# Performance work log

Measured on AMD Instinct MI355X. Metric: run time of the kernel, lower is better.

The kernel has to match this reference:

```python
import jax, jax.numpy as jnp
import numpy as np

N_NODES = 16384
N_EDGES = 32768
D = 128          # node feature / hidden dim
EDGE_DIM = 10    # bond featurizer one-hot dim
EH = 32          # edge_hidden_dim in the NNConv MLPs


def _nnconv(x, src, dst, edge_attr, l1w, l1b, l2w, l2b, root, bias):
    """PyG NNConv with aggr='mean': out_i = x_i @ root + mean_{e: dst=i} x_{src_e} @ W(e) + bias."""
    E = edge_attr.shape[0]
    h = jax.nn.relu(edge_attr @ l1w + l1b)              # [E, EH]
    W = (h @ l2w + l2b).reshape(E, D, D)                # per-edge weight matrices [E, D, D]
    msg = jnp.einsum('ei,eio->eo', x[src], W)           # gather + per-edge matmul [E, D]
    s = jax.ops.segment_sum(msg, dst, num_segments=N_NODES)
    cnt = jax.ops.segment_sum(jnp.ones((E, 1), x.dtype), dst, num_segments=N_NODES)
    agg = s / jnp.maximum(cnt, 1.0)                     # scatter-mean (0 for isolated nodes)
    return x @ root + agg + bias


def setup_inputs() -> dict:
    key = jax.random.key(0)
    ks = jax.random.split(key, 14)
    x = jax.random.normal(ks[0], (N_NODES, D), dtype=jnp.float32)
    edge_index = jax.random.randint(ks[1], (2, N_EDGES), 0, N_NODES, dtype=jnp.int64)
    edge_attr = jax.random.uniform(ks[2], (N_EDGES, EDGE_DIM), dtype=jnp.float32)

    def lin(k, fan_in, fan_out):
        return jax.random.normal(k, (fan_in, fan_out), dtype=jnp.float32) / np.sqrt(fan_in)

    return {
        'x': x, 'edge_index': edge_index, 'edge_attr': edge_attr,
        # subgraph_conv1 (128 -> 128)
        'w1_l1': lin(ks[3], EDGE_DIM, EH), 'b1_l1': jnp.zeros((EH,), jnp.float32),
        'w1_l2': lin(ks[4], EH, D * D),    'b1_l2': jnp.zeros((D * D,), jnp.float32),
        'w1_root': lin(ks[5], D, D),       'b1': jnp.zeros((D,), jnp.float32),
        # subgraph_conv2 (128 -> 128), applied twice with shared weights
        'w2_l1': lin(ks[6], EDGE_DIM, EH), 'b2_l1': jnp.zeros((EH,), jnp.float32),
        'w2_l2': lin(ks[7], EH, D * D),    'b2_l2': jnp.zeros((D * D,), jnp.float32),
        'w2_root': lin(ks[8], D, D),       'b2': jnp.zeros((D,), jnp.float32),
    }


def reference(x, edge_index, edge_attr,
              w1_l1, b1_l1, w1_l2, b1_l2, w1_root, b1,
              w2_l1, b2_l1, w2_l2, b2_l2, w2_root, b2):
    src, dst = edge_index[0], edge_index[1]
    h = jax.nn.relu(_nnconv(x, src, dst, edge_attr, w1_l1, b1_l1, w1_l2, b1_l2, w1_root, b1))
    h = jax.nn.relu(_nnconv(h, src, dst, edge_attr, w2_l1, b2_l1, w2_l2, b2_l2, w2_root, b2))
    h = _nnconv(h, src, dst, edge_attr, w2_l1, b2_l1, w2_l2, b2_l2, w2_root, b2)
    return h
```

## Files before the change

kernel.cpp:

```cpp
#include <hip/hip_runtime.h>

#define N_NODES 16384
#define N_EDGES 32768
#define D 128
#define EDGE_DIM 10
#define KH 32
#define BM 128
#define XST 136
#define NBL 32

typedef _Float16 f16;
typedef _Float16 f16x4 __attribute__((ext_vector_type(4)));
typedef _Float16 f16x8 __attribute__((ext_vector_type(8)));
typedef float f32x4 __attribute__((ext_vector_type(4)));

__global__ __launch_bounds__(256) void deg_count_kernel(
    const int* __restrict__ ei, int* __restrict__ deg) {
  int e = blockIdx.x * blockDim.x + threadIdx.x;
  if (e < N_EDGES) atomicAdd(&deg[ei[N_EDGES + e]], 1);
}

__global__ __launch_bounds__(1024) void scan_kernel(
    const int* __restrict__ deg, int* __restrict__ rs, int* __restrict__ fill) {
  __shared__ int part[1024];
  int t = threadIdx.x;
  int base = t * 16;
  int loc[16], s = 0;
#pragma unroll
  for (int j = 0; j < 16; j++) { loc[j] = deg[base + j]; s += loc[j]; }
  part[t] = s;
  __syncthreads();
  for (int off = 1; off < 1024; off <<= 1) {
    int add = (t >= off) ? part[t - off] : 0;
    __syncthreads();
    part[t] += add;
    __syncthreads();
  }
  int run = t ? part[t - 1] : 0;
#pragma unroll
  for (int j = 0; j < 16; j++) {
    rs[base + j] = run; fill[base + j] = run; run += loc[j];
  }
  if (t == 1023) rs[N_NODES] = run;
}

__global__ __launch_bounds__(256) void scatter_mlp_kernel(
    const int* __restrict__ ei, const float* __restrict__ ea,
    int* __restrict__ fill,
    const float* __restrict__ w1l1, const float* __restrict__ b1l1,
    const float* __restrict__ w2l1, const float* __restrict__ b2l1,
    int* __restrict__ srcs, f16* __restrict__ h1, f16* __restrict__ h2) {
  int e = blockIdx.x * blockDim.x + threadIdx.x;
  if (e >= N_EDGES) return;
  int pos = atomicAdd(&fill[ei[N_EDGES + e]], 1);
  srcs[pos] = ei[e];
  float a[EDGE_DIM];
#pragma unroll
  for (int d = 0; d < EDGE_DIM; d++) a[d] = ea[e * EDGE_DIM + d];
  f16 hv1[KH], hv2[KH];
#pragma unroll
  for (int k = 0; k < KH; k++) {
    float acc1 = b1l1[k], acc2 = b2l1[k];
#pragma unroll
    for (int d = 0; d < EDGE_DIM; d++) {
      acc1 += a[d] * w1l1[d * KH + k];
      acc2 += a[d] * w2l1[d * KH + k];
    }
    hv1[k] = (f16)fmaxf(acc1, 0.0f);
    hv2[k] = (f16)fmaxf(acc2, 0.0f);
  }
  f16x8* d1 = (f16x8*)(h1 + (size_t)pos * KH);
  f16x8* d2 = (f16x8*)(h2 + (size_t)pos * KH);
#pragma unroll
  for (int c = 0; c < 4; c++) {
    d1[c] = *(f16x8*)&hv1[c * 8];
    d2[c] = *(f16x8*)&hv2[c * 8];
  }
}

__global__ __launch_bounds__(256) void pack_all_kernel(
    const float* __restrict__ w1l2, const float* __restrict__ w2l2,
    const float* __restrict__ b1l2, const float* __restrict__ b2l2,
    const float* __restrict__ rt1, const float* __restrict__ rt2,
    f16* __restrict__ Bp1, f16* __restrict__ Bp2,
    f16* __restrict__ Rp1, f16* __restrict__ Rp2) {
  int y = blockIdx.y;
  int t = blockIdx.x * 256 + threadIdx.x;
  if (y < 2) {
    const float* l2w = y ? w2l2 : w1l2;
    f16* Bp = y ? Bp2 : Bp1;
    f16 tmp[KH];
#pragma unroll
    for (int k = 0; k < KH; k++) tmp[k] = (f16)l2w[(size_t)k * (D * D) + t];
    f16x8* dst = (f16x8*)(Bp + (size_t)t * KH);
#pragma unroll
    for (int c = 0; c < 4; c++) dst[c] = *(f16x8*)&tmp[c * 8];
  } else {
    const float* src = (y == 2) ? b1l2 : (y == 3) ? b2l2 : (y == 4) ? rt1 : rt2;
    f16* dst = (y == 2) ? (Bp1 + (size_t)D * D * KH)
             : (y == 3) ? (Bp2 + (size_t)D * D * KH)
             : (y == 4) ? Rp1 : Rp2;
    int i = t >> 7, o = t & 127;
    dst[((size_t)(i >> 5) * D + o) * KH + (i & 31)] = (f16)src[t];
  }
}

__global__ __launch_bounds__(256, 2) void msg_mfma_kernel(
    const float* __restrict__ xin, const f16* __restrict__ hf,
    const f16* __restrict__ Bp, const int* __restrict__ srcs,
    f16* __restrict__ msgf) {
  __shared__ f16 Xs[BM][XST];
  __shared__ f16 Hs[BM][KH];
  int t = threadIdx.x;
  int e0 = blockIdx.x * BM;

  ((f16x8*)Hs)[t] = ((const f16x8*)(hf + (size_t)e0 * KH))[t];
  ((f16x8*)Hs)[t + 256] = ((const f16x8*)(hf + (size_t)e0 * KH))[t + 256];
  {
    int r = t >> 1, q = t & 1;
    int s = srcs[e0 + r];
    const float4* src = (const float4*)(xin + (size_t)s * D + q * 64);
    f16* dst = &Xs[r][q * 64];
#pragma unroll
    for (int c = 0; c < 16; c++) {
      float4 v = src[c];
      f16x4 h4 = {(f16)v.x, (f16)v.y, (f16)v.z, (f16)v.w};
      *(f16x4*)(dst + c * 4) = h4;
    }
  }

  int L = t & 63, w = t >> 6;
  int quad = L >> 4, lm = L & 15;
  int n0 = blockIdx.y * 64 + w * 16;

  const f16* bl = Bp + (size_t)(n0 + lm) * KH + quad * 8;
  const size_t istr = (size_t)D * KH;

  f32x4 acc[8];
#pragma unroll
  for (int mt = 0; mt < 8; mt++) acc[mt] = (f32x4){0.f, 0.f, 0.f, 0.f};

  f16x8 bufA[8], bufB[8];

  auto loadg = [&](f16x8 (&buf)[8], int basei) {
#pragma unroll
    for (int jj = 0; jj < 8; jj++)
      buf[jj] = *(const f16x8*)(bl + (size_t)(basei + jj) * istr);
  };

  f16x8 hreg[8];

  auto compute = [&](f16x8 (&buf)[8], int ig) {
    f16x8 xv[8];
#pragma unroll
    for (int mt = 0; mt < 8; mt++)
      xv[mt] = *(const f16x8*)&Xs[mt * 16 + lm][ig];
#pragma unroll
    for (int jj = 0; jj < 8; jj++) {
#pragma unroll
      for (int mt = 0; mt < 8; mt++) {
        f16 xs = xv[mt][jj];
        f16x8 xb = {xs, xs, xs, xs, xs, xs, xs, xs};
        f16x8 a = hreg[mt] * xb;
        acc[mt] = __builtin_amdgcn_mfma_f32_16x16x32_f16(a, buf[jj], acc[mt], 0, 0, 0);
      }
    }
  };

  loadg(bufA, 0);
  __syncthreads();

#pragma unroll
  for (int mt = 0; mt < 8; mt++)
    hreg[mt] = *(const f16x8*)&Hs[mt * 16 + lm][quad * 8];

#pragma unroll 1
  for (int g = 0; g < 8; g++) {
    loadg(bufB, 16 * g + 8);
    compute(bufA, 16 * g);
    loadg(bufA, 16 * g + 16);
    compute(bufB, 16 * g + 8);
  }

#pragma unroll
  for (int ig2 = 0; ig2 < 4; ig2++) {
#pragma unroll
    for (int mt = 0; mt < 8; mt++) {
      f16x8 a = *(const f16x8*)&Xs[mt * 16 + lm][ig2 * 32 + quad * 8];
      acc[mt] = __builtin_amdgcn_mfma_f32_16x16x32_f16(a, bufA[ig2], acc[mt], 0, 0, 0);
    }
  }

#pragma unroll
  for (int mt = 0; mt < 8; mt++)
#pragma unroll
    for (int r = 0; r < 4; r++)
      msgf[(size_t)(e0 + mt * 16 + quad * 4 + r) * D + n0 + lm] = (f16)acc[mt][r];
}

__global__ __launch_bounds__(256) void node_update_kernel(
    const float* __restrict__ xin, const f16* __restrict__ msgf,
    const int* __restrict__ rs, const f16* __restrict__ Rp,
    const float* __restrict__ bias, float* __restrict__ out, int do_relu) {
  __shared__ f16 Xs[NBL][XST];
  __shared__ float Sls[NBL][D];
  int t = threadIdx.x;
  int nb = blockIdx.x * NBL;

  {
    int r = t >> 3, q = t & 7;
    const float4* src = (const float4*)(xin + (size_t)(nb + r) * D + q * 16);
    f16* dst = &Xs[r][q * 16];
#pragma unroll
    for (int c = 0; c < 4; c++) {
      float4 v = src[c];
      f16x4 h4 = {(f16)v.x, (f16)v.y, (f16)v.z, (f16)v.w};
      *(f16x4*)(dst + c * 4) = h4;
    }
  }
  __syncthreads();

  {
    int nl = t >> 3, o0 = (t & 7) * 16;
    int n = nb + nl;
    int a = rs[n], b = rs[n + 1];
    float sum[16];
#pragma unroll
    for (int j = 0; j < 16; j++) sum[j] = 0.f;
    for (int r = a; r < b; r++) {
      f16x8 v0 = *(const f16x8*)(msgf + (size_t)r * D + o0);
      f16x8 v1 = *(const f16x8*)(msgf + (size_t)r * D + o0 + 8);
#pragma unroll
      for (int j = 0; j < 8; j++) {
        sum[j] += (float)v0[j];
        sum[8 + j] += (float)v1[j];
      }
    }
    float inv = 1.0f / (float)max(b - a, 1);
#pragma unroll
    for (int j = 0; j < 16; j++) Sls[nl][o0 + j] = sum[j] * inv;
  }
  __syncthreads();

  int L = t & 63, w = t >> 6;
  int quad = L >> 4, lm = L & 15;
  int n0 = w * 32;
  f32x4 acc[2][2];
#pragma unroll
  for (int mt = 0; mt < 2; mt++)
#pragma unroll
    for (int nt = 0; nt < 2; nt++)
      acc[mt][nt] = (f32x4){0.f, 0.f, 0.f, 0.f};
#pragma unroll
  for (int s4 = 0; s4 < 4; s4++) {
    const f16* b2l = Rp + ((size_t)s4 * D + n0 + lm) * KH + quad * 8;
    f16x8 b0 = *(const f16x8*)b2l;
    f16x8 b1 = *(const f16x8*)(b2l + 16 * KH);
#pragma unroll
    for (int mt = 0; mt < 2; mt++) {
      f16x8 a = *(const f16x8*)&Xs[mt * 16 + lm][s4 * 32 + quad * 8];
      acc[mt][0] = __builtin_amdgcn_mfma_f32_16x16x32_f16(a, b0, acc[mt][0], 0, 0, 0);
      acc[mt][1] = __builtin_amdgcn_mfma_f32_16x16x32_f16(a, b1, acc[mt][1], 0, 0, 0);
    }
  }
#pragma unroll
  for (int mt = 0; mt < 2; mt++)
#pragma unroll
    for (int r = 0; r < 4; r++) {
      Sls[mt * 16 + quad * 4 + r][n0 + lm] += acc[mt][0][r];
      Sls[mt * 16 + quad * 4 + r][n0 + 16 + lm] += acc[mt][1][r];
    }
  __syncthreads();

  {
    int o = t & 127, g = t >> 7;
    float bo = bias[o];
    for (int q = g * 16; q < g * 16 + 16; q++) {
      float v = bo + Sls[q][o];
      out[(size_t)(nb + q) * D + o] = do_relu ? fmaxf(v, 0.0f) : v;
    }
  }
}

extern "C" void kernel_launch(void* const* d_in, const int* in_sizes, int n_in,
                              void* d_out, int out_size, void* d_ws, size_t ws_size,
                              hipStream_t stream) {
  const float* x      = (const float*)d_in[0];
  const int*   ei     = (const int*)d_in[1];
  const float* ea     = (const float*)d_in[2];
  const float* w1_l1  = (const float*)d_in[3];
  const float* b1_l1  = (const float*)d_in[4];
  const float* w1_l2  = (const float*)d_in[5];
  const float* b1_l2  = (const float*)d_in[6];
  const float* w1_rt  = (const float*)d_in[7];
  const float* b1     = (const float*)d_in[8];
  const float* w2_l1  = (const float*)d_in[9];
  const float* b2_l1  = (const float*)d_in[10];
  const float* w2_l2  = (const float*)d_in[11];
  const float* b2_l2  = (const float*)d_in[12];
  const float* w2_rt  = (const float*)d_in[13];
  const float* b2     = (const float*)d_in[14];
  float* out = (float*)d_out;

  const size_t BPSZ = (size_t)D * D * KH + (size_t)D * D;
  f16* h1f = (f16*)d_ws;
  f16* h2f = h1f + (size_t)N_EDGES * KH;
  f16* Bp1 = h2f + (size_t)N_EDGES * KH;
  f16* Bp2 = Bp1 + BPSZ;
  f16* Rp1 = Bp2 + BPSZ;
  f16* Rp2 = Rp1 + (size_t)D * D;
  int* deg  = (int*)(Rp2 + (size_t)D * D);
  int* rs   = deg + N_NODES;
  int* fill = rs + N_NODES + 128;
  int* srcs = fill + N_NODES;
  f16* msgf = (f16*)(srcs + N_EDGES);

  hipMemsetAsync(deg, 0, N_NODES * sizeof(int), stream);
  deg_count_kernel<<<N_EDGES / 256, 256, 0, stream>>>(ei, deg);
  scan_kernel<<<1, 1024, 0, stream>>>(deg, rs, fill);
  scatter_mlp_kernel<<<N_EDGES / 256, 256, 0, stream>>>(
      ei, ea, fill, w1_l1, b1_l1, w2_l1, b2_l1, srcs, h1f, h2f);
  pack_all_kernel<<<dim3(D * D / 256, 6), 256, 0, stream>>>(
      w1_l2, w2_l2, b1_l2, b2_l2, w1_rt, w2_rt, Bp1, Bp2, Rp1, Rp2);

  msg_mfma_kernel<<<dim3(N_EDGES / BM, 2), 256, 0, stream>>>(x, h1f, Bp1, srcs, msgf);
  node_update_kernel<<<N_NODES / NBL, 256, 0, stream>>>(x, msgf, rs, Rp1, b1, out, 1);
  msg_mfma_kernel<<<dim3(N_EDGES / BM, 2), 256, 0, stream>>>(out, h2f, Bp2, srcs, msgf);
  node_update_kernel<<<N_NODES / NBL, 256, 0, stream>>>(out, msgf, rs, Rp2, b2, out, 1);
  msg_mfma_kernel<<<dim3(N_EDGES / BM, 2), 256, 0, stream>>>(out, h2f, Bp2, srcs, msgf);
  node_update_kernel<<<N_NODES / NBL, 256, 0, stream>>>(out, msgf, rs, Rp2, b2, out, 0);
}
```

Measured before the change: 276.6 us.

## Split message kernel over input-dim halves with two partial message buffers

The message kernel now splits the reduction (input) dimension across blockIdx.y instead of the output dimension. Each block computes all 128 outputs for half of the inputs, writing partial messages to two separate buffers that the node update kernel sums. This halves the gathered X tile in shared memory and reuses each broadcast-scaled A operand across two MFMAs, at the cost of doubling message write and read traffic. The degree count and weight packing kernels are also merged into one launch.

```diff
diff --git a/kernel.cpp b/kernel.cpp
--- a/kernel.cpp
+++ b/kernel.cpp
@@ -6,6 +6,7 @@
 #define EDGE_DIM 10
 #define KH 32
 #define BM 128
+#define XST2 72
 #define XST 136
 #define NBL 32
 
@@ -14,10 +15,39 @@
 typedef _Float16 f16x8 __attribute__((ext_vector_type(8)));
 typedef float f32x4 __attribute__((ext_vector_type(4)));
 
-__global__ __launch_bounds__(256) void deg_count_kernel(
-    const int* __restrict__ ei, int* __restrict__ deg) {
-  int e = blockIdx.x * blockDim.x + threadIdx.x;
-  if (e < N_EDGES) atomicAdd(&deg[ei[N_EDGES + e]], 1);
+__global__ __launch_bounds__(256) void deg_pack_kernel(
+    const int* __restrict__ ei, int* __restrict__ deg,
+    const float* __restrict__ w1l2, const float* __restrict__ w2l2,
+    const float* __restrict__ b1l2, const float* __restrict__ b2l2,
+    const float* __restrict__ rt1, const float* __restrict__ rt2,
+    f16* __restrict__ Bp1, f16* __restrict__ Bp2,
+    f16* __restrict__ Rp1, f16* __restrict__ Rp2) {
+  int y = blockIdx.y;
+  if (y == 0) {
+    int e = blockIdx.x * 256 + threadIdx.x;
+    if (e < N_EDGES) atomicAdd(&deg[ei[N_EDGES + e]], 1);
+    return;
+  }
+  if (blockIdx.x >= D * D / 256) return;
+  int t = blockIdx.x * 256 + threadIdx.x;
+  int j = y - 1;
+  if (j < 2) {
+    const float* l2w = j ? w2l2 : w1l2;
+    f16* Bp = j ? Bp2 : Bp1;
+    f16 tmp[KH];
+#pragma unroll
+    for (int k = 0; k < KH; k++) tmp[k] = (f16)l2w[(size_t)k * (D * D) + t];
+    f16x8* dst = (f16x8*)(Bp + (size_t)t * KH);
+#pragma unroll
+    for (int c = 0; c < 4; c++) dst[c] = *(f16x8*)&tmp[c * 8];
+  } else {
+    const float* src = (j == 2) ? b1l2 : (j == 3) ? b2l2 : (j == 4) ? rt1 : rt2;
+    f16* dst = (j == 2) ? (Bp1 + (size_t)D * D * KH)
+             : (j == 3) ? (Bp2 + (size_t)D * D * KH)
+             : (j == 4) ? Rp1 : Rp2;
+    int i = t >> 7, o = t & 127;
+    dst[((size_t)(i >> 5) * D + o) * KH + (i & 31)] = (f16)src[t];
+  }
 }
 
 __global__ __launch_bounds__(1024) void scan_kernel(
@@ -78,51 +108,26 @@
   }
 }
 
-__global__ __launch_bounds__(256) void pack_all_kernel(
-    const float* __restrict__ w1l2, const float* __restrict__ w2l2,
-    const float* __restrict__ b1l2, const float* __restrict__ b2l2,
-    const float* __restrict__ rt1, const float* __restrict__ rt2,
-    f16* __restrict__ Bp1, f16* __restrict__ Bp2,
-    f16* __restrict__ Rp1, f16* __restrict__ Rp2) {
-  int y = blockIdx.y;
-  int t = blockIdx.x * 256 + threadIdx.x;
-  if (y < 2) {
-    const float* l2w = y ? w2l2 : w1l2;
-    f16* Bp = y ? Bp2 : Bp1;
-    f16 tmp[KH];
-#pragma unroll
-    for (int k = 0; k < KH; k++) tmp[k] = (f16)l2w[(size_t)k * (D * D) + t];
-    f16x8* dst = (f16x8*)(Bp + (size_t)t * KH);
-#pragma unroll
-    for (int c = 0; c < 4; c++) dst[c] = *(f16x8*)&tmp[c * 8];
-  } else {
-    const float* src = (y == 2) ? b1l2 : (y == 3) ? b2l2 : (y == 4) ? rt1 : rt2;
-    f16* dst = (y == 2) ? (Bp1 + (size_t)D * D * KH)
-             : (y == 3) ? (Bp2 + (size_t)D * D * KH)
-             : (y == 4) ? Rp1 : Rp2;
-    int i = t >> 7, o = t & 127;
-    dst[((size_t)(i >> 5) * D + o) * KH + (i & 31)] = (f16)src[t];
-  }
-}
-
 __global__ __launch_bounds__(256, 2) void msg_mfma_kernel(
     const float* __restrict__ xin, const f16* __restrict__ hf,
     const f16* __restrict__ Bp, const int* __restrict__ srcs,
-    f16* __restrict__ msgf) {
-  __shared__ f16 Xs[BM][XST];
+    f16* __restrict__ msgfA, f16* __restrict__ msgfB) {
+  __shared__ f16 Xs[BM][XST2];
   __shared__ f16 Hs[BM][KH];
   int t = threadIdx.x;
   int e0 = blockIdx.x * BM;
-
-  ((f16x8*)Hs)[t] = ((const f16x8*)(hf + (size_t)e0 * KH))[t];
+  int y  = blockIdx.y;
+  f16* msgf = y ? msgfB : msgfA;
+
+  ((f16x8*)Hs)[t]       = ((const f16x8*)(hf + (size_t)e0 * KH))[t];
   ((f16x8*)Hs)[t + 256] = ((const f16x8*)(hf + (size_t)e0 * KH))[t + 256];
   {
     int r = t >> 1, q = t & 1;
     int s = srcs[e0 + r];
-    const float4* src = (const float4*)(xin + (size_t)s * D + q * 64);
-    f16* dst = &Xs[r][q * 64];
-#pragma unroll
-    for (int c = 0; c < 16; c++) {
+    const float4* src = (const float4*)(xin + (size_t)s * D + y * 64 + q * 32);
+    f16* dst = &Xs[r][q * 32];
+#pragma unroll
+    for (int c = 0; c < 8; c++) {
       float4 v = src[c];
       f16x4 h4 = {(f16)v.x, (f16)v.y, (f16)v.z, (f16)v.w};
       *(f16x4*)(dst + c * 4) = h4;
@@ -131,38 +136,45 @@
 
   int L = t & 63, w = t >> 6;
   int quad = L >> 4, lm = L & 15;
-  int n0 = blockIdx.y * 64 + w * 16;
-
-  const f16* bl = Bp + (size_t)(n0 + lm) * KH + quad * 8;
+  int n0 = w * 32;
+
+  const f16* bl = Bp + ((size_t)(y * 64) * D + n0 + lm) * KH + quad * 8;
   const size_t istr = (size_t)D * KH;
 
-  f32x4 acc[8];
-#pragma unroll
-  for (int mt = 0; mt < 8; mt++) acc[mt] = (f32x4){0.f, 0.f, 0.f, 0.f};
-
-  f16x8 bufA[8], bufB[8];
-
-  auto loadg = [&](f16x8 (&buf)[8], int basei) {
-#pragma unroll
-    for (int jj = 0; jj < 8; jj++)
-      buf[jj] = *(const f16x8*)(bl + (size_t)(basei + jj) * istr);
+  f32x4 acc[8][2];
+#pragma unroll
+  for (int mt = 0; mt < 8; mt++)
+#pragma unroll
+    for (int nt = 0; nt < 2; nt++)
+      acc[mt][nt] = (f32x4){0.f, 0.f, 0.f, 0.f};
+
+  f16x8 bufA[4][2], bufB[4][2];
+
+  auto loadg = [&](f16x8 (&buf)[4][2], int basei) {
+#pragma unroll
+    for (int jj = 0; jj < 4; jj++) {
+      const f16* bi = bl + (size_t)(basei + jj) * istr;
+      buf[jj][0] = *(const f16x8*)bi;
+      buf[jj][1] = *(const f16x8*)(bi + 16 * KH);
+    }
   };
 
   f16x8 hreg[8];
 
-  auto compute = [&](f16x8 (&buf)[8], int ig) {
-    f16x8 xv[8];
+  auto compute = [&](f16x8 (&buf)[4][2], int ig) {
+    f16x4 xv[8];
 #pragma unroll
     for (int mt = 0; mt < 8; mt++)
-      xv[mt] = *(const f16x8*)&Xs[mt * 16 + lm][ig];
-#pragma unroll
-    for (int jj = 0; jj < 8; jj++) {
+      xv[mt] = *(const f16x4*)&Xs[mt * 16 + lm][ig];
+#pragma unroll
+    for (int jj = 0; jj < 4; jj++) {
 #pragma unroll
       for (int mt = 0; mt < 8; mt++) {
         f16 xs = xv[mt][jj];
         f16x8 xb = {xs, xs, xs, xs, xs, xs, xs, xs};
         f16x8 a = hreg[mt] * xb;
-        acc[mt] = __builtin_amdgcn_mfma_f32_16x16x32_f16(a, buf[jj], acc[mt], 0, 0, 0);
+        acc[mt][0] = __builtin_amdgcn_mfma_f32_16x16x32_f16(a, buf[jj][0], acc[mt][0], 0, 0, 0);
+        acc[mt][1] = __builtin_amdgcn_mfma_f32_16x16x32_f16(a, buf[jj][1], acc[mt][1], 0, 0, 0);
       }
     }
   };
@@ -176,32 +188,45 @@
 
 #pragma unroll 1
   for (int g = 0; g < 8; g++) {
-    loadg(bufB, 16 * g + 8);
-    compute(bufA, 16 * g);
-    loadg(bufA, 16 * g + 16);
-    compute(bufB, 16 * g + 8);
-  }
-
-#pragma unroll
-  for (int ig2 = 0; ig2 < 4; ig2++) {
-#pragma unroll
-    for (int mt = 0; mt < 8; mt++) {
-      f16x8 a = *(const f16x8*)&Xs[mt * 16 + lm][ig2 * 32 + quad * 8];
-      acc[mt] = __builtin_amdgcn_mfma_f32_16x16x32_f16(a, bufA[ig2], acc[mt], 0, 0, 0);
+    loadg(bufB, 8 * g + 4);
+    compute(bufA, 8 * g);
+    loadg(bufA, 8 * g + 8);
+    compute(bufB, 8 * g + 4);
+  }
+
+  {
+    const f16* bb = Bp + (size_t)D * D * KH;
+#pragma unroll
+    for (int g2 = 0; g2 < 2; g2++) {
+      int ig2 = 2 * y + g2;
+      const f16* b2l = bb + ((size_t)ig2 * D + n0 + lm) * KH + quad * 8;
+      f16x8 b0 = *(const f16x8*)b2l;
+      f16x8 b1 = *(const f16x8*)(b2l + 16 * KH);
+      int lc = g2 * 32 + quad * 8;
+#pragma unroll
+      for (int mt = 0; mt < 8; mt++) {
+        f16x8 a = *(const f16x8*)&Xs[mt * 16 + lm][lc];
+        acc[mt][0] = __builtin_amdgcn_mfma_f32_16x16x32_f16(a, b0, acc[mt][0], 0, 0, 0);
+        acc[mt][1] = __builtin_amdgcn_mfma_f32_16x16x32_f16(a, b1, acc[mt][1], 0, 0, 0);
+      }
     }
   }
 
 #pragma unroll
   for (int mt = 0; mt < 8; mt++)
 #pragma unroll
-    for (int r = 0; r < 4; r++)
-      msgf[(size_t)(e0 + mt * 16 + quad * 4 + r) * D + n0 + lm] = (f16)acc[mt][r];
+    for (int r = 0; r < 4; r++) {
+      f16* mg = msgf + (size_t)(e0 + mt * 16 + quad * 4 + r) * D + n0 + lm;
+      mg[0]  = (f16)acc[mt][0][r];
+      mg[16] = (f16)acc[mt][1][r];
+    }
 }
 
 __global__ __launch_bounds__(256) void node_update_kernel(
-    const float* __restrict__ xin, const f16* __restrict__ msgf,
-    const int* __restrict__ rs, const f16* __restrict__ Rp,
-    const float* __restrict__ bias, float* __restrict__ out, int do_relu) {
+    const float* __restrict__ xin, const f16* __restrict__ msgA,
+    const f16* __restrict__ msgB, const int* __restrict__ rs,
+    const f16* __restrict__ Rp, const float* __restrict__ bias,
+    float* __restrict__ out, int do_relu) {
   __shared__ f16 Xs[NBL][XST];
   __shared__ float Sls[NBL][D];
   int t = threadIdx.x;
@@ -228,12 +253,14 @@
 #pragma unroll
     for (int j = 0; j < 16; j++) sum[j] = 0.f;
     for (int r = a; r < b; r++) {
-      f16x8 v0 = *(const f16x8*)(msgf + (size_t)r * D + o0);
-      f16x8 v1 = *(const f16x8*)(msgf + (size_t)r * D + o0 + 8);
+      f16x8 a0 = *(const f16x8*)(msgA + (size_t)r * D + o0);
+      f16x8 a1 = *(const f16x8*)(msgA + (size_t)r * D + o0 + 8);
+      f16x8 b0 = *(const f16x8*)(msgB + (size_t)r * D + o0);
+      f16x8 b1 = *(const f16x8*)(msgB + (size_t)r * D + o0 + 8);
 #pragma unroll
       for (int j = 0; j < 8; j++) {
-        sum[j] += (float)v0[j];
-        sum[8 + j] += (float)v1[j];
+        sum[j]     += (float)a0[j] + (float)b0[j];
+        sum[8 + j] += (float)a1[j] + (float)b1[j];
       }
     }
     float inv = 1.0f / (float)max(b - a, 1);
@@ -302,7 +329,7 @@
   const float* b2     = (const float*)d_in[14];
   float* out = (float*)d_out;
 
-  const size_t BPSZ = (size_t)D * D * KH + (size_t)D * D;
+  const size_t BPSZ = (size_t)D * D * KH + (size_t)D * D + 32768;
   f16* h1f = (f16*)d_ws;
   f16* h2f = h1f + (size_t)N_EDGES * KH;
   f16* Bp1 = h2f + (size_t)N_EDGES * KH;
@@ -313,20 +340,20 @@
   int* rs   = deg + N_NODES;
   int* fill = rs + N_NODES + 128;
   int* srcs = fill + N_NODES;
-  f16* msgf = (f16*)(srcs + N_EDGES);
+  f16* msgA = (f16*)(srcs + N_EDGES);
+  f16* msgB = msgA + (size_t)N_EDGES * D;
 
   hipMemsetAsync(deg, 0, N_NODES * sizeof(int), stream);
-  deg_count_kernel<<<N_EDGES / 256, 256, 0, stream>>>(ei, deg);
+  deg_pack_kernel<<<dim3(N_EDGES / 256, 7), 256, 0, stream>>>(
+      ei, deg, w1_l2, w2_l2, b1_l2, b2_l2, w1_rt, w2_rt, Bp1, Bp2, Rp1, Rp2);
   scan_kernel<<<1, 1024, 0, stream>>>(deg, rs, fill);
   scatter_mlp_kernel<<<N_EDGES / 256, 256, 0, stream>>>(
       ei, ea, fill, w1_l1, b1_l1, w2_l1, b2_l1, srcs, h1f, h2f);
-  pack_all_kernel<<<dim3(D * D / 256, 6), 256, 0, stream>>>(
-      w1_l2, w2_l2, b1_l2, b2_l2, w1_rt, w2_rt, Bp1, Bp2, Rp1, Rp2);
-
-  msg_mfma_kernel<<<dim3(N_EDGES / BM, 2), 256, 0, stream>>>(x, h1f, Bp1, srcs, msgf);
-  node_update_kernel<<<N_NODES / NBL, 256, 0, stream>>>(x, msgf, rs, Rp1, b1, out, 1);
-  msg_mfma_kernel<<<dim3(N_EDGES / BM, 2), 256, 0, stream>>>(out, h2f, Bp2, srcs, msgf);
-  node_update_kernel<<<N_NODES / NBL, 256, 0, stream>>>(out, msgf, rs, Rp2, b2, out, 1);
-  msg_mfma_kernel<<<dim3(N_EDGES / BM, 2), 256, 0, stream>>>(out, h2f, Bp2, srcs, msgf);
-  node_update_kernel<<<N_NODES / NBL, 256, 0, stream>>>(out, msgf, rs, Rp2, b2, out, 0);
-}
+
+  msg_mfma_kernel<<<dim3(N_EDGES / BM, 2), 256, 0, stream>>>(x, h1f, Bp1, srcs, msgA, msgB);
+  node_update_kernel<<<N_NODES / NBL, 256, 0, stream>>>(x, msgA, msgB, rs, Rp1, b1, out, 1);
+  msg_mfma_kernel<<<dim3(N_EDGES / BM, 2), 256, 0, stream>>>(out, h2f, Bp2, srcs, msgA, msgB);
+  node_update_kernel<<<N_NODES / NBL, 256, 0, stream>>>(out, msgA, msgB, rs, Rp2, b2, out, 1);
+  msg_mfma_kernel<<<dim3(N_EDGES / BM, 2), 256, 0, stream>>>(out, h2f, Bp2, srcs, msgA, msgB);
+  node_update_kernel<<<N_NODES / NBL, 256, 0, stream>>>(out, msgA, msgB, rs, Rp2, b2, out, 0);
+}
```

Result: faster. 257.7 us (-6.8%).
